# Kernel tuning notes

Measured on AMD Instinct MI355X. Metric: run time of the kernel, lower is better.

## Reference

```python
import jax, jax.numpy as jnp
import numpy as np

EPS = 1e-6

def elu_fm(x):
    # elu(x) + 1
    return jax.nn.elu(x) + 1.0

def setup_inputs() -> dict:
    key = jax.random.key(0)
    k1, k2, k3 = jax.random.split(key, 3)
    N, L, H, D = 4, 4096, 16, 64
    queries = jax.random.normal(k1, (N, L, H, D), dtype=jnp.float32)
    keys = jax.random.normal(k2, (N, L, H, D), dtype=jnp.float32)
    values = jax.random.normal(k3, (N, L, H, D), dtype=jnp.float32)
    key_mask = jnp.ones((N, L), dtype=jnp.float32)
    return {"queries": queries, "keys": keys, "values": values, "key_mask": key_mask}

def reference(queries, keys, values, key_mask):
    Q = elu_fm(queries)                                  # [n, l, h, d]
    K = elu_fm(keys) * key_mask[:, :, None, None]        # [n, s, h, d]
    # KV accumulation: outer products of keys and values summed over sequence
    KV = jnp.einsum('nshd,nshm->nhmd', K, values)        # [n, h, m, d]
    # Normalizer: Q . sum_s K
    Z = 1.0 / (jnp.einsum('nlhd,nhd->nlh', Q, K.sum(axis=1)) + EPS)
    V = jnp.einsum('nlhd,nhmd,nlh->nlhm', Q, KV, Z)      # [n, l, h, m]
    return V
```

## Files before the change

kernel.cpp:

```cpp
#include <hip/hip_runtime.h>

#define EPS 1e-6f

typedef __attribute__((ext_vector_type(8))) short short8;
typedef __attribute__((ext_vector_type(16))) float f32x16;

__device__ __forceinline__ float elu1(float x) {
    return x > 0.f ? x + 1.f : __expf(x);
}

__device__ __forceinline__ short f2bf(float x) {
    unsigned u = __float_as_uint(x);
    return (short)((u + 0x7FFFu + ((u >> 16) & 1u)) >> 16);
}

__device__ __forceinline__ void gl16(const float* g, float* l) {
    __builtin_amdgcn_global_load_lds(
        (const __attribute__((address_space(1))) unsigned int*)g,
        (__attribute__((address_space(3))) unsigned int*)l, 16, 0, 0);
}

#define VMCNT(n) asm volatile("s_waitcnt vmcnt(" #n ")" ::: "memory")
#define LGKMCNT0() asm volatile("s_waitcnt lgkmcnt(0)" ::: "memory")

__global__ __launch_bounds__(64) void kv_partial_kernel(
    const float* __restrict__ keys, const float* __restrict__ values,
    const float* __restrict__ mask, float* __restrict__ pkv,
    float* __restrict__ pks, int steps)
{
    __shared__ float Kls[2][16][64];
    __shared__ float Vls[2][16][64];

    const int nh = blockIdx.x;
    const int n = nh >> 4, h = nh & 15;
    const int chunk = blockIdx.y;
    const int l = threadIdx.x;
    const int half = l >> 5, col = l & 31;

    const int s0 = chunk * steps * 16;
    const float* kb = keys   + ((size_t)(n * 4096 + s0) * 16 + h) * 64;
    const float* vb = values + ((size_t)(n * 4096 + s0) * 16 + h) * 64;
    const float* mb = mask + n * 4096 + s0 + 8 * half;

    const size_t lanerow = (size_t)(l >> 4) * 1024 + (size_t)(l & 15) * 4;

    f32x16 acc[2][2];
    #pragma unroll
    for (int a = 0; a < 2; ++a)
        #pragma unroll
        for (int b = 0; b < 2; ++b)
            #pragma unroll
            for (int r = 0; r < 16; ++r) acc[a][b][r] = 0.f;

    float ks0 = 0.f, ks1 = 0.f;
    float4 mA0, mA1, mB0, mB1;

#define ISSUE(st, p)                                                      \
    { _Pragma("unroll")                                                   \
      for (int q = 0; q < 4; ++q) {                                       \
          const size_t go = (size_t)((st) * 16 + 4 * q) * 1024 + lanerow; \
          gl16(kb + go, &Kls[p][4 * q][0]);                               \
          gl16(vb + go, &Vls[p][4 * q][0]);                               \
      } }

#define MASKLD(st, m0, m1)                                                \
    { m0 = *(const float4*)(mb + (st) * 16);                              \
      m1 = *(const float4*)(mb + (st) * 16 + 4); }

#define COMPUTE(p, m0, m1)                                                \
    { short8 ka0, ka1, va0, va1;                                          \
      const float mm[8] = {m0.x, m0.y, m0.z, m0.w, m1.x, m1.y, m1.z, m1.w}; \
      _Pragma("unroll")                                                   \
      for (int j = 0; j < 8; ++j) {                                       \
          const int s = 8 * half + j;                                     \
          const float k0 = elu1(Kls[p][s][col]) * mm[j];                  \
          const float k1 = elu1(Kls[p][s][col + 32]) * mm[j];             \
          ks0 += k0; ks1 += k1;                                           \
          ka0[j] = f2bf(k0); ka1[j] = f2bf(k1);                           \
          va0[j] = f2bf(Vls[p][s][col]);                                  \
          va1[j] = f2bf(Vls[p][s][col + 32]);                             \
      }                                                                   \
      LGKMCNT0();                                                         \
      acc[0][0] = __builtin_amdgcn_mfma_f32_32x32x16_bf16(ka0, va0, acc[0][0], 0, 0, 0); \
      acc[0][1] = __builtin_amdgcn_mfma_f32_32x32x16_bf16(ka0, va1, acc[0][1], 0, 0, 0); \
      acc[1][0] = __builtin_amdgcn_mfma_f32_32x32x16_bf16(ka1, va0, acc[1][0], 0, 0, 0); \
      acc[1][1] = __builtin_amdgcn_mfma_f32_32x32x16_bf16(ka1, va1, acc[1][1], 0, 0, 0); \
    }

    ISSUE(0, 0); MASKLD(0, mA0, mA1);
    ISSUE(1, 1); MASKLD(1, mB0, mB1);
    VMCNT(10);

    for (int st = 0; st < steps; st += 2) {
        COMPUTE(0, mA0, mA1);
        if (st + 2 < steps) { ISSUE(st + 2, 0); MASKLD(st + 2, mA0, mA1); VMCNT(10); }
        else { VMCNT(0); }
        COMPUTE(1, mB0, mB1);
        if (st + 3 < steps) { ISSUE(st + 3, 1); MASKLD(st + 3, mB0, mB1); VMCNT(10); }
        else { VMCNT(0); }
    }
#undef ISSUE
#undef MASKLD
#undef COMPUTE

    ks0 += __shfl_xor(ks0, 32);
    ks1 += __shfl_xor(ks1, 32);
    pks[((size_t)chunk * 64 + nh) * 64 + l] = half ? ks1 : ks0;

    float* pb = pkv + ((size_t)chunk * 64 + nh) * 4096;
    #pragma unroll
    for (int td = 0; td < 2; ++td)
        #pragma unroll
        for (int tm = 0; tm < 2; ++tm)
            #pragma unroll
            for (int r = 0; r < 16; ++r) {
                const int d = 32 * td + (r & 3) + 8 * (r >> 2) + 4 * half;
                pb[(size_t)d * 64 + 32 * tm + col] = acc[td][tm][r];
            }
}

__global__ __launch_bounds__(256) void kv_reduce_kernel(
    const float* __restrict__ pkv, const float* __restrict__ pks,
    float* __restrict__ kvt, float* __restrict__ ksum, int CH)
{
    const int nh = blockIdx.x;
    const int f4 = blockIdx.y * 256 + threadIdx.x;
    float4 s4 = make_float4(0.f, 0.f, 0.f, 0.f);
    #pragma unroll 4
    for (int c = 0; c < CH; ++c) {
        const float4 v = *(const float4*)(pkv + ((size_t)c * 64 + nh) * 4096 + f4 * 4);
        s4.x += v.x; s4.y += v.y; s4.z += v.z; s4.w += v.w;
    }
    *(float4*)(kvt + (size_t)nh * 4096 + f4 * 4) = s4;

    if (blockIdx.y == 0 && threadIdx.x < 64) {
        float s = 0.f;
        #pragma unroll 4
        for (int c = 0; c < CH; ++c)
            s += pks[((size_t)c * 64 + nh) * 64 + threadIdx.x];
        ksum[nh * 64 + threadIdx.x] = s;
    }
}

__global__ __launch_bounds__(256) void out_kernel(
    const float* __restrict__ queries, const float* __restrict__ kvt,
    const float* __restrict__ ksum, float* __restrict__ out)
{
    __shared__ float Qs[64][68];
    __shared__ float KVs[64][68];
    __shared__ float Ksm[64];

    const int nh = blockIdx.x;
    const int n = nh >> 4, h = nh & 15;
    const int t = threadIdx.x;
    const int l0 = blockIdx.y * 64;

    #pragma unroll
    for (int k = 0; k < 4; ++k) {
        const int idx = t + k * 256;
        *(float4*)&KVs[idx >> 4][(idx & 15) * 4] =
            *(const float4*)(kvt + (size_t)nh * 4096 + idx * 4);
    }
    if (t < 64) Ksm[t] = ksum[nh * 64 + t];

    #pragma unroll
    for (int k = 0; k < 4; ++k) {
        const int idx = t + k * 256;
        const int row = idx >> 4, seg = idx & 15;
        const size_t g = ((size_t)(n * 4096 + l0 + row) * 16 + h) * 64 + seg * 4;
        float4 q4 = *(const float4*)(queries + g);
        q4.x = elu1(q4.x);
        q4.y = elu1(q4.y);
        q4.z = elu1(q4.z);
        q4.w = elu1(q4.w);
        *(float4*)&Qs[row][seg * 4] = q4;
    }
    __syncthreads();

    const int mg = t & 7;
    const int lg = t >> 3;

    float acc[2][8];
    float zacc[2] = {0.f, 0.f};
    #pragma unroll
    for (int i = 0; i < 2; ++i)
        #pragma unroll
        for (int j = 0; j < 8; ++j) acc[i][j] = 0.f;

    #pragma unroll 4
    for (int d0 = 0; d0 < 64; d0 += 4) {
        const float4 km4 = *(const float4*)&Ksm[d0];
        float4 q[2];
        q[0] = *(const float4*)&Qs[lg][d0];
        q[1] = *(const float4*)&Qs[lg + 32][d0];
        #pragma unroll
        for (int i = 0; i < 2; ++i)
            zacc[i] += q[i].x * km4.x + q[i].y * km4.y +
                       q[i].z * km4.z + q[i].w * km4.w;
        #pragma unroll
        for (int r = 0; r < 4; ++r) {
            const float4 kva = *(const float4*)&KVs[d0 + r][mg * 4];
            const float4 kvb = *(const float4*)&KVs[d0 + r][32 + mg * 4];
            #pragma unroll
            for (int i = 0; i < 2; ++i) {
                const float qc = ((const float*)&q[i])[r];
                acc[i][0] = fmaf(qc, kva.x, acc[i][0]);
                acc[i][1] = fmaf(qc, kva.y, acc[i][1]);
                acc[i][2] = fmaf(qc, kva.z, acc[i][2]);
                acc[i][3] = fmaf(qc, kva.w, acc[i][3]);
                acc[i][4] = fmaf(qc, kvb.x, acc[i][4]);
                acc[i][5] = fmaf(qc, kvb.y, acc[i][5]);
                acc[i][6] = fmaf(qc, kvb.z, acc[i][6]);
                acc[i][7] = fmaf(qc, kvb.w, acc[i][7]);
            }
        }
    }

    #pragma unroll
    for (int i = 0; i < 2; ++i) {
        const float z = 1.f / (zacc[i] + EPS);
        const int row = l0 + lg + 32 * i;
        const size_t g = ((size_t)(n * 4096 + row) * 16 + h) * 64;
        float4 o;
        o.x = acc[i][0] * z; o.y = acc[i][1] * z;
        o.z = acc[i][2] * z; o.w = acc[i][3] * z;
        *(float4*)(out + g + mg * 4) = o;
        o.x = acc[i][4] * z; o.y = acc[i][5] * z;
        o.z = acc[i][6] * z; o.w = acc[i][7] * z;
        *(float4*)(out + g + 32 + mg * 4) = o;
    }
}

extern "C" void kernel_launch(void* const* d_in, const int* in_sizes, int n_in,
                              void* d_out, int out_size, void* d_ws, size_t ws_size,
                              hipStream_t stream) {
    const float* queries = (const float*)d_in[0];
    const float* keys    = (const float*)d_in[1];
    const float* values  = (const float*)d_in[2];
    const float* mask    = (const float*)d_in[3];
    float* out = (float*)d_out;

    int CH = 32;
    while (CH > 2) {
        size_t need = ((size_t)CH * 64 * 4096 + (size_t)CH * 64 * 64 +
                       (size_t)64 * 4096 + 64 * 64) * sizeof(float);
        if (need <= ws_size) break;
        CH >>= 1;
    }
    const int steps = 4096 / (CH * 16);

    float* pkv  = (float*)d_ws;
    float* pks  = pkv + (size_t)CH * 64 * 4096;
    float* kvt  = pks + (size_t)CH * 64 * 64;
    float* ksum = kvt + (size_t)64 * 4096;

    kv_partial_kernel<<<dim3(64, CH), 64, 0, stream>>>(keys, values, mask,
                                                       pkv, pks, steps);
    kv_reduce_kernel<<<dim3(64, 4), 256, 0, stream>>>(pkv, pks, kvt, ksum, CH);
    out_kernel<<<dim3(64, 64), 256, 0, stream>>>(queries, kvt, ksum, out);
}
```

Baseline: 88.73 us.

## Process all 16 heads per block with cooperative triple-buffered sequence loads

```diff
diff --git a/kernel.cpp b/kernel.cpp
--- a/kernel.cpp
+++ b/kernel.cpp
@@ -23,26 +23,29 @@
 #define VMCNT(n) asm volatile("s_waitcnt vmcnt(" #n ")" ::: "memory")
 #define LGKMCNT0() asm volatile("s_waitcnt lgkmcnt(0)" ::: "memory")
 
-__global__ __launch_bounds__(64) void kv_partial_kernel(
+template<int NW>
+__global__ __launch_bounds__(1024, 1) void kv_partial_kernel(
     const float* __restrict__ keys, const float* __restrict__ values,
     const float* __restrict__ mask, float* __restrict__ pkv,
-    float* __restrict__ pks, int steps)
+    float* __restrict__ pks)
 {
-    __shared__ float Kls[2][16][64];
-    __shared__ float Vls[2][16][64];
-
-    const int nh = blockIdx.x;
-    const int n = nh >> 4, h = nh & 15;
-    const int chunk = blockIdx.y;
-    const int l = threadIdx.x;
+    __shared__ float SB[3][2][2][1024];
+    __shared__ float Mls[128];
+
+    const int chunk = blockIdx.x, n = blockIdx.y;
+    const int t = threadIdx.x;
+    const int wv = t >> 6, l = t & 63;
     const int half = l >> 5, col = l & 31;
-
-    const int s0 = chunk * steps * 16;
-    const float* kb = keys   + ((size_t)(n * 4096 + s0) * 16 + h) * 64;
-    const float* vb = values + ((size_t)(n * 4096 + s0) * 16 + h) * 64;
-    const float* mb = mask + n * 4096 + s0 + 8 * half;
-
-    const size_t lanerow = (size_t)(l >> 4) * 1024 + (size_t)(l & 15) * 4;
+    const int s0 = chunk * (NW * 16);
+
+    const float* kb = keys   + (size_t)(n * 4096 + s0) * 1024;
+    const float* vb = values + (size_t)(n * 4096 + s0) * 1024;
+
+    const int arr = wv & 1, rsel = (wv >> 1) & 1, seg = wv >> 2;
+    const float* src = arr ? vb : kb;
+    const int laneoff = seg * 256 + l * 4;
+
+    if (t < NW * 16) Mls[t] = mask[n * 4096 + s0 + t];
 
     f32x16 acc[2][2];
     #pragma unroll
@@ -53,58 +56,47 @@
             for (int r = 0; r < 16; ++r) acc[a][b][r] = 0.f;
 
     float ks0 = 0.f, ks1 = 0.f;
-    float4 mA0, mA1, mB0, mB1;
-
-#define ISSUE(st, p)                                                      \
-    { _Pragma("unroll")                                                   \
-      for (int q = 0; q < 4; ++q) {                                       \
-          const size_t go = (size_t)((st) * 16 + 4 * q) * 1024 + lanerow; \
-          gl16(kb + go, &Kls[p][4 * q][0]);                               \
-          gl16(vb + go, &Vls[p][4 * q][0]);                               \
-      } }
-
-#define MASKLD(st, m0, m1)                                                \
-    { m0 = *(const float4*)(mb + (st) * 16);                              \
-      m1 = *(const float4*)(mb + (st) * 16 + 4); }
-
-#define COMPUTE(p, m0, m1)                                                \
-    { short8 ka0, ka1, va0, va1;                                          \
-      const float mm[8] = {m0.x, m0.y, m0.z, m0.w, m1.x, m1.y, m1.z, m1.w}; \
-      _Pragma("unroll")                                                   \
-      for (int j = 0; j < 8; ++j) {                                       \
-          const int s = 8 * half + j;                                     \
-          const float k0 = elu1(Kls[p][s][col]) * mm[j];                  \
-          const float k1 = elu1(Kls[p][s][col + 32]) * mm[j];             \
-          ks0 += k0; ks1 += k1;                                           \
-          ka0[j] = f2bf(k0); ka1[j] = f2bf(k1);                           \
-          va0[j] = f2bf(Vls[p][s][col]);                                  \
-          va1[j] = f2bf(Vls[p][s][col + 32]);                             \
-      }                                                                   \
-      LGKMCNT0();                                                         \
-      acc[0][0] = __builtin_amdgcn_mfma_f32_32x32x16_bf16(ka0, va0, acc[0][0], 0, 0, 0); \
-      acc[0][1] = __builtin_amdgcn_mfma_f32_32x32x16_bf16(ka0, va1, acc[0][1], 0, 0, 0); \
-      acc[1][0] = __builtin_amdgcn_mfma_f32_32x32x16_bf16(ka1, va0, acc[1][0], 0, 0, 0); \
-      acc[1][1] = __builtin_amdgcn_mfma_f32_32x32x16_bf16(ka1, va1, acc[1][1], 0, 0, 0); \
-    }
-
-    ISSUE(0, 0); MASKLD(0, mA0, mA1);
-    ISSUE(1, 1); MASKLD(1, mB0, mB1);
-    VMCNT(10);
-
-    for (int st = 0; st < steps; st += 2) {
-        COMPUTE(0, mA0, mA1);
-        if (st + 2 < steps) { ISSUE(st + 2, 0); MASKLD(st + 2, mA0, mA1); VMCNT(10); }
-        else { VMCNT(0); }
-        COMPUTE(1, mB0, mB1);
-        if (st + 3 < steps) { ISSUE(st + 3, 1); MASKLD(st + 3, mB0, mB1); VMCNT(10); }
-        else { VMCNT(0); }
+    short8 ka0, ka1, va0, va1;
+
+#define ISSUE(ST)                                                          \
+    { const int row_ = ((ST) >> 3) * 16 + ((ST) & 7) + 8 * rsel;           \
+      gl16(src + (size_t)row_ * 1024 + laneoff,                            \
+           &SB[(ST) % 3][arr][rsel][seg * 256]); }
+
+    ISSUE(0);
+    ISSUE(1);
+    LGKMCNT0();
+    __builtin_amdgcn_s_barrier();
+
+    #pragma unroll
+    for (int w = 0; w < NW; ++w) {
+        #pragma unroll
+        for (int q = 0; q < 8; ++q) {
+            const int st = w * 8 + q;
+            VMCNT(1);
+            __builtin_amdgcn_s_barrier();
+            if (st + 2 < NW * 8) ISSUE(st + 2);
+            const float msk = Mls[w * 16 + q + 8 * half];
+            const float* Kp = &SB[st % 3][0][half][wv * 64];
+            const float* Vp = &SB[st % 3][1][half][wv * 64];
+            const float k0 = elu1(Kp[col]) * msk;
+            const float k1 = elu1(Kp[col + 32]) * msk;
+            ks0 += k0; ks1 += k1;
+            ka0[q] = f2bf(k0); ka1[q] = f2bf(k1);
+            va0[q] = f2bf(Vp[col]); va1[q] = f2bf(Vp[col + 32]);
+            if (q == 7) {
+                acc[0][0] = __builtin_amdgcn_mfma_f32_32x32x16_bf16(ka0, va0, acc[0][0], 0, 0, 0);
+                acc[0][1] = __builtin_amdgcn_mfma_f32_32x32x16_bf16(ka0, va1, acc[0][1], 0, 0, 0);
+                acc[1][0] = __builtin_amdgcn_mfma_f32_32x32x16_bf16(ka1, va0, acc[1][0], 0, 0, 0);
+                acc[1][1] = __builtin_amdgcn_mfma_f32_32x32x16_bf16(ka1, va1, acc[1][1], 0, 0, 0);
+            }
+        }
     }
 #undef ISSUE
-#undef MASKLD
-#undef COMPUTE
 
     ks0 += __shfl_xor(ks0, 32);
     ks1 += __shfl_xor(ks1, 32);
+    const int nh = n * 16 + wv;
     pks[((size_t)chunk * 64 + nh) * 64 + l] = half ? ks1 : ks0;
 
     float* pb = pkv + ((size_t)chunk * 64 + nh) * 4096;
@@ -240,22 +232,21 @@
     const float* mask    = (const float*)d_in[3];
     float* out = (float*)d_out;
 
-    int CH = 32;
-    while (CH > 2) {
-        size_t need = ((size_t)CH * 64 * 4096 + (size_t)CH * 64 * 64 +
-                       (size_t)64 * 4096 + 64 * 64) * sizeof(float);
-        if (need <= ws_size) break;
-        CH >>= 1;
-    }
-    const int steps = 4096 / (CH * 16);
+    auto need = [](int CH) {
+        return ((size_t)CH * 64 * 4096 + (size_t)CH * 64 * 64 +
+                (size_t)64 * 4096 + 64 * 64) * sizeof(float);
+    };
+    const int CH = (need(64) <= ws_size) ? 64 : 32;
 
     float* pkv  = (float*)d_ws;
     float* pks  = pkv + (size_t)CH * 64 * 4096;
     float* kvt  = pks + (size_t)CH * 64 * 64;
     float* ksum = kvt + (size_t)64 * 4096;
 
-    kv_partial_kernel<<<dim3(64, CH), 64, 0, stream>>>(keys, values, mask,
-                                                       pkv, pks, steps);
+    if (CH == 64)
+        kv_partial_kernel<4><<<dim3(64, 4), 1024, 0, stream>>>(keys, values, mask, pkv, pks);
+    else
+        kv_partial_kernel<8><<<dim3(32, 4), 1024, 0, stream>>>(keys, values, mask, pkv, pks);
     kv_reduce_kernel<<<dim3(64, 4), 256, 0, stream>>>(pkv, pks, kvt, ksum, CH);
     out_kernel<<<dim3(64, 64), 256, 0, stream>>>(queries, kvt, ksum, out);
 }
```

Measured after the change: 116.2 us. +31.0%, slower.
